# Kernel optimization log

Measured on AMD Instinct MI355X. Metric: run time of the kernel, lower is better.

Reference implementation:

```python
import jax, jax.numpy as jnp
import numpy as np

B, S, D = 4, 4096, 1024
H = 16
DH = D // H  # 64, required by the fused kernel


def setup_inputs() -> dict:
    key = jax.random.key(0)
    ks = jax.random.split(key, 5)
    scale = 1.0 / np.sqrt(D)  # xavier-ish init scale for square matrices
    return {
        "x": jax.random.normal(ks[0], (B, S, D), dtype=jnp.float32),
        "Wq": jax.random.normal(ks[1], (D, D), dtype=jnp.float32) * scale,
        "Wk": jax.random.normal(ks[2], (D, D), dtype=jnp.float32) * scale,
        "Wv": jax.random.normal(ks[3], (D, D), dtype=jnp.float32) * scale,
        "Wo": jax.random.normal(ks[4], (D, D), dtype=jnp.float32) * scale,
    }


def reference(x, Wq, Wk, Wv, Wo):
    # Fused QKV projection + linear (non-softmax) attention.
    # Q = x Wq, K = x Wk, V = x Wv, split into H heads of size DH.
    b, s, d = x.shape
    h, dh = H, d // H

    def to_heads(t):
        return t.reshape(b, s, h, dh).transpose(0, 2, 1, 3)  # [B,H,S,dh]

    q = to_heads(jnp.einsum("bsd,de->bse", x, Wq))
    k = to_heads(jnp.einsum("bsd,de->bse", x, Wk))
    v = to_heads(jnp.einsum("bsd,de->bse", x, Wv))

    # Linear attention: O(S * dh^2) per head, never materializes [S,S].
    # out = (1/sqrt(dh)) * Q @ (K^T V)
    scale = 1.0 / jnp.sqrt(jnp.asarray(dh, dtype=x.dtype))
    kv = jnp.einsum("bhsd,bhse->bhde", k, v)          # [B,H,dh,dh]
    out = jnp.einsum("bhsd,bhde->bhse", q, kv) * scale  # [B,H,S,dh]

    # kernel output [B,H,S,dh] -> transpose(1,2) -> view [B,S,D]
    out = out.transpose(0, 2, 1, 3).reshape(b, s, d)
    # out_proj: nn.Linear(D, D, bias=False) -> x @ W.T
    return jnp.einsum("bsd,ed->bse", out, Wo)
```

## Files before the change

### kernel.cpp

```cpp
#include <hip/hip_runtime.h>

typedef unsigned short u16;
typedef unsigned int u32;
typedef u16 u16x8 __attribute__((ext_vector_type(8)));
typedef u16 u16x4 __attribute__((ext_vector_type(4)));
typedef __bf16 bf16x8 __attribute__((ext_vector_type(8)));
typedef float f32x4 __attribute__((ext_vector_type(4)));

__device__ __forceinline__ u16 f2bf(float f) {
    u32 u = __builtin_bit_cast(u32, f);
    u32 r = (u + 0x7fffu + ((u >> 16) & 1u)) >> 16;
    return (u16)r;
}
__device__ __forceinline__ void async16(const u16* g, u16* lds_base) {
    __builtin_amdgcn_global_load_lds(
        (const __attribute__((address_space(1))) void*)g,
        (__attribute__((address_space(3))) void*)lds_base, 16, 0, 0);
}
__device__ __forceinline__ void storeC(float* p, float v) { *p = v; }
__device__ __forceinline__ void storeC(u16* p, float v)   { *p = f2bf(v); }

__global__ void cvt_f32_bf16(const float* __restrict__ in, u16* __restrict__ out, long n) {
    long idx = ((long)blockIdx.x * blockDim.x + threadIdx.x) * 8;
    if (idx >= n) return;
    float4 a = *(const float4*)(in + idx);
    float4 b = *(const float4*)(in + idx + 4);
    u16x8 o;
    o[0] = f2bf(a.x); o[1] = f2bf(a.y); o[2] = f2bf(a.z); o[3] = f2bf(a.w);
    o[4] = f2bf(b.x); o[5] = f2bf(b.y); o[6] = f2bf(b.z); o[7] = f2bf(b.w);
    *(u16x8*)(out + idx) = o;
}

__global__ void transpose_cvt(const float* __restrict__ W0, const float* __restrict__ W1,
                              u16* __restrict__ WT) {
    __shared__ float tile[32][33];
    const float* W = (blockIdx.z == 0) ? W0 : W1;
    int n0 = blockIdx.x * 32, k0 = blockIdx.y * 32;
    int tx = threadIdx.x, ty = threadIdx.y;
#pragma unroll
    for (int r = 0; r < 4; ++r)
        tile[ty + 8 * r][tx] = W[(size_t)(k0 + ty + 8 * r) * 1024 + n0 + tx];
    __syncthreads();
#pragma unroll
    for (int r = 0; r < 4; ++r) {
        int n = n0 + ty + 8 * r;
        WT[((size_t)blockIdx.z * 1024 + n) * 1024 + k0 + tx] = f2bf(tile[tx][ty + 8 * r]);
    }
}

#define BAR __builtin_amdgcn_s_barrier()
#define WAITLGK do { asm volatile("s_waitcnt lgkmcnt(0)" ::: "memory"); \
                     __builtin_amdgcn_sched_barrier(0); } while (0)
#define PRIO1 __builtin_amdgcn_s_setprio(1)
#define PRIO0 __builtin_amdgcn_s_setprio(0)
#define VM(n) asm volatile("s_waitcnt vmcnt(" #n ")" ::: "memory")

#define As SM[0]
#define Bs SM[1]

#define LDA(buf, mh) do { _Pragma("unroll") for (int mi = 0; mi < 4; ++mi) { \
    const int rA = (wm * 128 + (mh) * 64 + mi * 16 + frow) * 64; \
    aF[mi][0] = *(const bf16x8*)&As[buf][rA + xs0]; \
    aF[mi][1] = *(const bf16x8*)&As[buf][rA + xs1]; } } while (0)

#define LDB(buf, nh) do { _Pragma("unroll") for (int ni = 0; ni < 2; ++ni) { \
    const int rB = (wn * 64 + (nh) * 32 + ni * 16 + frow) * 64; \
    bF[(nh) * 2 + ni][0] = *(const bf16x8*)&Bs[buf][rB + xs0]; \
    bF[(nh) * 2 + ni][1] = *(const bf16x8*)&Bs[buf][rB + xs1]; } } while (0)

#define MFQ(mh, nh) do { _Pragma("unroll") for (int mi = 0; mi < 4; ++mi) \
  _Pragma("unroll") for (int ni = 0; ni < 2; ++ni) \
  _Pragma("unroll") for (int s = 0; s < 2; ++s) \
    acc[(mh) * 4 + mi][(nh) * 2 + ni] = __builtin_amdgcn_mfma_f32_16x16x32_bf16( \
        aF[mi][s], bF[(nh) * 2 + ni][s], acc[(mh) * 4 + mi][(nh) * 2 + ni], 0, 0, 0); } while (0)

#define TILE4(buf, S1, S2, S3, S4, WV) \
  LDA(buf, 0); LDB(buf, 0); S1; BAR; WAITLGK; PRIO1; MFQ(0, 0); PRIO0; BAR; \
  LDB(buf, 1); S2; BAR; WAITLGK; PRIO1; MFQ(0, 1); PRIO0; BAR; \
  LDA(buf, 1); S3; BAR; WAITLGK; PRIO1; MFQ(1, 1); PRIO0; BAR; \
  S4; BAR; WAITLGK; PRIO1; MFQ(1, 0); PRIO0; WV; BAR;

template <typename OutT, bool KVMODE>
__global__ __launch_bounds__(512, 2) void gemm8p(
    const u16* __restrict__ A, int lda,
    const u16* __restrict__ Bt, int ldb,
    OutT* __restrict__ Cq, int ldc, int K, int nTN,
    size_t btStrideB, u16* __restrict__ Kt, u16* __restrict__ Vt) {
    __shared__ u16 SM[2][2][256 * 64];
    const int tid = threadIdx.x;
    const int wid = tid >> 6, lane = tid & 63;
    const int wm = wid >> 2, wn = wid & 3;

    const int nwg = gridDim.x;
    const int orig = blockIdx.x;
    const int id = (orig & 7) * (nwg >> 3) + (orig >> 3);
    const size_t mBase = (size_t)(id / nTN) * 256;
    const size_t nBase = (size_t)(id % nTN) * 256;

    if (!KVMODE) Bt += (mBase >> 12) * btStrideB;

    const int srow = lane >> 3;
    const int scol = (((lane & 7) ^ (srow & 7)) * 8);

    auto stageH = [&](int buf, int isB, int h, int kt) {
        const u16* g = isB ? Bt : A;
        const int ld = isB ? ldb : lda;
        const size_t rb = isB ? nBase : mBase;
        u16* lds = isB ? Bs[buf] : As[buf];
#pragma unroll
        for (int j = 0; j < 2; ++j) {
            const int rowL = isB ? ((wid >> 1) * 64 + h * 32 + (wid & 1) * 16 + j * 8)
                                 : ((wid >> 2) * 128 + h * 64 + (wid & 3) * 16 + j * 8);
            async16(g + (rb + rowL + srow) * (size_t)ld + (size_t)kt * 64 + scol,
                    lds + rowL * 64);
        }
    };

    const int frow = lane & 15;
    const int xs0 = (((lane >> 4)) ^ (frow & 7)) * 8;
    const int xs1 = ((4 + (lane >> 4)) ^ (frow & 7)) * 8;

    f32x4 acc[8][4] = {};
    bf16x8 aF[4][2], bF[4][2];

#pragma unroll
    for (int h = 0; h < 2; ++h) { stageH(0, 0, h, 0); stageH(0, 1, h, 0); }
#pragma unroll
    for (int h = 0; h < 2; ++h) { stageH(1, 0, h, 1); stageH(1, 1, h, 1); }
    VM(8);
    BAR;

    const int np = K >> 7;
    for (int p = 0; p < np - 1; ++p) {
        const int k2 = 2 * p + 2, k3 = 2 * p + 3;
        TILE4(0, ,
              { stageH(0, 0, 0, k2); stageH(0, 1, 0, k2); },
              stageH(0, 1, 1, k2),
              stageH(0, 0, 1, k2),
              VM(8));
        TILE4(1, ,
              { stageH(1, 0, 0, k3); stageH(1, 1, 0, k3); },
              stageH(1, 1, 1, k3),
              stageH(1, 0, 1, k3),
              VM(8));
    }
    TILE4(0, , , , , VM(0));
    TILE4(1, , , , , );

    const int rb4 = (lane >> 4) * 4;
    const int cx = lane & 15;
    if (!KVMODE) {
#pragma unroll
        for (int m = 0; m < 8; ++m) {
#pragma unroll
            for (int n = 0; n < 4; ++n) {
                const size_t col = nBase + wn * 64 + n * 16 + cx;
#pragma unroll
                for (int r = 0; r < 4; ++r) {
                    const size_t row = mBase + wm * 128 + m * 16 + rb4 + r;
                    storeC(&Cq[row * (size_t)ldc + col], acc[m][n][r]);
                }
            }
        }
    } else {
        __syncthreads();
        u16* T = &SM[0][0][0];
        const int nLoc = (int)(nBase & 1023);
#pragma unroll
        for (int n = 0; n < 4; ++n) {
            const int colL = wn * 64 + n * 16 + cx;
#pragma unroll
            for (int m = 0; m < 8; ++m) {
                const int R = wm * 128 + m * 16 + rb4;
                u16x4 v;
                v[0] = f2bf(acc[m][n][0]); v[1] = f2bf(acc[m][n][1]);
                v[2] = f2bf(acc[m][n][2]); v[3] = f2bf(acc[m][n][3]);
                const int byteoff = colL * 512 + ((((R >> 3) ^ (colL & 31)) << 4) | ((R & 7) << 1));
                *(u16x4*)((char*)T + byteoff) = v;
            }
        }
        __syncthreads();
        const int b = (int)(mBase >> 12);
        u16* KV = ((nBase >> 10) == 0 ? Kt : Vt);
        const int j = lane & 31;
#pragma unroll
        for (int u = 0; u < 16; ++u) {
            const int iLoc = wid * 32 + u * 2 + (lane >> 5);
            const int byteoff = iLoc * 512 + ((j ^ (iLoc & 31)) << 4);
            const int gcol = nLoc + iLoc;
            u16* dst = KV + (((size_t)(b * 16 + (gcol >> 6)) * 64 + (gcol & 63)) << 12)
                          + (mBase & 4095) + j * 8;
            *(u16x8*)dst = *(const u16x8*)((char*)T + byteoff);
        }
    }
}

__global__ __launch_bounds__(256, 2) void gemm128(
    const u16* __restrict__ A, int lda,
    const u16* __restrict__ Bt, int ldb,
    u16* __restrict__ C, int ldc, int K) {
    __shared__ u16 A2[2][128 * 64];
    __shared__ u16 B2[2][128 * 64];
    const int tid = threadIdx.x, w = tid >> 6, lane = tid & 63;
    const int wr = w >> 1, wc = w & 1;
    const size_t mBase = (size_t)blockIdx.y * 128;
    const size_t nBase = (size_t)blockIdx.x * 128;
    const int lr = lane >> 3;
    const int scol = ((lane & 7) ^ lr) * 8;

    auto stage = [&](int buf, int kt) {
#pragma unroll
        for (int c = 0; c < 2; ++c) {
            const u16* g = c ? Bt : A;
            const int ld = c ? ldb : lda;
            const size_t rb = c ? nBase : mBase;
            u16* lds = c ? B2[buf] : A2[buf];
#pragma unroll
            for (int jj = 0; jj < 4; ++jj) {
                const int rowL = jj * 32 + w * 8;
                async16(g + (rb + rowL + lr) * (size_t)ld + (size_t)kt * 64 + scol,
                        lds + rowL * 64);
            }
        }
    };

    const int frow = lane & 15;
    const int xs0 = ((lane >> 4) ^ (frow & 7)) * 8;
    const int xs1 = ((4 + (lane >> 4)) ^ (frow & 7)) * 8;
    f32x4 acc[4][4] = {};

    stage(0, 0);
    __syncthreads();
    const int nk = K >> 6;
    for (int kt = 0; kt < nk; ++kt) {
        const int cur = kt & 1;
        if (kt + 1 < nk) stage(cur ^ 1, kt + 1);
        bf16x8 bF[4][2];
#pragma unroll
        for (int n = 0; n < 4; ++n) {
            const int rB = (wc * 64 + n * 16 + frow) * 64;
            bF[n][0] = *(const bf16x8*)&B2[cur][rB + xs0];
            bF[n][1] = *(const bf16x8*)&B2[cur][rB + xs1];
        }
#pragma unroll
        for (int m = 0; m < 4; ++m) {
            const int rA = (wr * 64 + m * 16 + frow) * 64;
            bf16x8 a0 = *(const bf16x8*)&A2[cur][rA + xs0];
            bf16x8 a1 = *(const bf16x8*)&A2[cur][rA + xs1];
#pragma unroll
            for (int n = 0; n < 4; ++n) {
                acc[m][n] = __builtin_amdgcn_mfma_f32_16x16x32_bf16(a0, bF[n][0], acc[m][n], 0, 0, 0);
                acc[m][n] = __builtin_amdgcn_mfma_f32_16x16x32_bf16(a1, bF[n][1], acc[m][n], 0, 0, 0);
            }
        }
        __syncthreads();
    }
    const int rb4 = (lane >> 4) * 4, cx = lane & 15;
#pragma unroll
    for (int m = 0; m < 4; ++m)
#pragma unroll
        for (int n = 0; n < 4; ++n) {
            const size_t col = nBase + wc * 64 + n * 16 + cx;
#pragma unroll
            for (int r = 0; r < 4; ++r)
                C[(mBase + wr * 64 + m * 16 + rb4 + r) * (size_t)ldc + col] = f2bf(acc[m][n][r]);
        }
}

__global__ __launch_bounds__(256, 2) void kv_gemm(
    const u16* __restrict__ Kt, const u16* __restrict__ Vt, float* __restrict__ P) {
    __shared__ u16 Ks[64 * 64];
    __shared__ u16 Vs[64 * 64];
    const int chunk = blockIdx.x, bh = blockIdx.y;
    const int tid = threadIdx.x, w = tid >> 6, lane = tid & 63;
    const int srow = lane >> 3;
    const int scol = ((lane & 7) ^ srow) * 8;
    const int frow = lane & 15;
    const int xs0 = ((lane >> 4) ^ (frow & 7)) * 8;
    const int xs1 = ((4 + (lane >> 4)) ^ (frow & 7)) * 8;
    const size_t base = (size_t)bh * 64 * 4096 + (size_t)chunk * 512;
    f32x4 acc[4] = {};
    for (int kk = 0; kk < 8; ++kk) {
        __syncthreads();
#pragma unroll
        for (int j = 0; j < 2; ++j) {
            const int row = w * 16 + j * 8;
            async16(Kt + base + (size_t)(row + srow) * 4096 + kk * 64 + scol, &Ks[row * 64]);
            async16(Vt + base + (size_t)(row + srow) * 4096 + kk * 64 + scol, &Vs[row * 64]);
        }
        asm volatile("s_waitcnt vmcnt(0)" ::: "memory");
        __syncthreads();
        bf16x8 a0 = *(const bf16x8*)&Ks[(w * 16 + frow) * 64 + xs0];
        bf16x8 a1 = *(const bf16x8*)&Ks[(w * 16 + frow) * 64 + xs1];
#pragma unroll
        for (int n = 0; n < 4; ++n) {
            bf16x8 b0 = *(const bf16x8*)&Vs[(n * 16 + frow) * 64 + xs0];
            bf16x8 b1 = *(const bf16x8*)&Vs[(n * 16 + frow) * 64 + xs1];
            acc[n] = __builtin_amdgcn_mfma_f32_16x16x32_bf16(a0, b0, acc[n], 0, 0, 0);
            acc[n] = __builtin_amdgcn_mfma_f32_16x16x32_bf16(a1, b1, acc[n], 0, 0, 0);
        }
    }
    const int rb4 = (lane >> 4) * 4, cx = lane & 15;
    float* p = P + ((size_t)chunk * 64 + bh) * 4096;
#pragma unroll
    for (int n = 0; n < 4; ++n)
#pragma unroll
        for (int r = 0; r < 4; ++r)
            p[(w * 16 + rb4 + r) * 64 + n * 16 + cx] = acc[n][r];
}

__global__ void kv_reduce(const float* __restrict__ P, u16* __restrict__ kvb) {
    const int bh = blockIdx.x, t = threadIdx.x;
    for (int idx = t; idx < 4096; idx += 256) {
        float s = 0.f;
#pragma unroll
        for (int c = 0; c < 8; ++c) s += P[((size_t)c * 64 + bh) * 4096 + idx];
        kvb[(size_t)bh * 4096 + idx] = f2bf(s * 0.125f);
    }
}

__global__ __launch_bounds__(256, 2) void w2_gemm(
    const u16* __restrict__ Wob, const u16* __restrict__ kvb, u16* __restrict__ W2t) {
    __shared__ u16 Aw[256 * 64];
    __shared__ u16 Bw[64 * 64];
    const int eT = blockIdx.x, h = blockIdx.y, b = blockIdx.z;
    const int tid = threadIdx.x, w = tid >> 6, lane = tid & 63;
    const int srow = lane >> 3;
    const int scol = ((lane & 7) ^ srow) * 8;
#pragma unroll
    for (int j = 0; j < 8; ++j) {
        const int row = w * 64 + j * 8;
        async16(Wob + (size_t)(eT * 256 + row + srow) * 1024 + h * 64 + scol, &Aw[row * 64]);
    }
#pragma unroll
    for (int j = 0; j < 2; ++j) {
        const int row = w * 16 + j * 8;
        async16(kvb + ((size_t)(b * 16 + h) * 64 + row + srow) * 64 + scol, &Bw[row * 64]);
    }
    asm volatile("s_waitcnt vmcnt(0)" ::: "memory");
    __syncthreads();
    const int frow = lane & 15;
    const int xs0 = ((lane >> 4) ^ (frow & 7)) * 8;
    const int xs1 = ((4 + (lane >> 4)) ^ (frow & 7)) * 8;
    f32x4 acc[4][4] = {};
#pragma unroll
    for (int m = 0; m < 4; ++m) {
        bf16x8 a0 = *(const bf16x8*)&Aw[(w * 64 + m * 16 + frow) * 64 + xs0];
        bf16x8 a1 = *(const bf16x8*)&Aw[(w * 64 + m * 16 + frow) * 64 + xs1];
#pragma unroll
        for (int n = 0; n < 4; ++n) {
            bf16x8 b0 = *(const bf16x8*)&Bw[(n * 16 + frow) * 64 + xs0];
            bf16x8 b1 = *(const bf16x8*)&Bw[(n * 16 + frow) * 64 + xs1];
            acc[m][n] = __builtin_amdgcn_mfma_f32_16x16x32_bf16(a0, b0, acc[m][n], 0, 0, 0);
            acc[m][n] = __builtin_amdgcn_mfma_f32_16x16x32_bf16(a1, b1, acc[m][n], 0, 0, 0);
        }
    }
    const int rb4 = (lane >> 4) * 4, cx = lane & 15;
    u16* out = W2t + (size_t)b * 1048576;
#pragma unroll
    for (int m = 0; m < 4; ++m)
#pragma unroll
        for (int n = 0; n < 4; ++n)
#pragma unroll
            for (int r = 0; r < 4; ++r)
                out[(size_t)(eT * 256 + w * 64 + m * 16 + rb4 + r) * 1024 + h * 64 + n * 16 + cx] =
                    f2bf(acc[m][n][r]);
}

extern "C" void kernel_launch(void* const* d_in, const int* in_sizes, int n_in,
                              void* d_out, int out_size, void* d_ws, size_t ws_size,
                              hipStream_t stream) {
    const float* x  = (const float*)d_in[0];
    const float* Wq = (const float*)d_in[1];
    const float* Wk = (const float*)d_in[2];
    const float* Wv = (const float*)d_in[3];
    const float* Wo = (const float*)d_in[4];
    float* out = (float*)d_out;
    char* ws = (char*)d_ws;

    u16*   xb    = (u16*)(ws);
    u16*   Kt    = (u16*)(ws + 33554432);
    u16*   Vt    = (u16*)(ws + 67108864);
    u16*   WkvT  = (u16*)(ws + 100663296);
    u16*   Wqb   = (u16*)(ws + 104857600);
    u16*   Wob   = (u16*)(ws + 106954752);
    float* Pkv   = (float*)(ws + 109051904);
    u16*   kvb   = (u16*)(ws + 117440512);
    u16*   W2t   = (u16*)(ws + 117964800);
    u16*   W3T   = (u16*)(ws + 126353408);

    cvt_f32_bf16<<<8192, 256, 0, stream>>>(x, xb, 16777216L);
    cvt_f32_bf16<<<512, 256, 0, stream>>>(Wq, Wqb, 1048576L);
    cvt_f32_bf16<<<512, 256, 0, stream>>>(Wo, Wob, 1048576L);
    transpose_cvt<<<dim3(32, 32, 2), dim3(32, 8), 0, stream>>>(Wk, Wv, WkvT);

    gemm8p<u16, true><<<512, 512, 0, stream>>>(xb, 1024, WkvT, 1024, (u16*)nullptr, 0,
                                               1024, 8, 0, Kt, Vt);

    kv_gemm<<<dim3(8, 64), 256, 0, stream>>>(Kt, Vt, Pkv);
    kv_reduce<<<64, 256, 0, stream>>>(Pkv, kvb);
    w2_gemm<<<dim3(4, 16, 4), 256, 0, stream>>>(Wob, kvb, W2t);

    gemm128<<<dim3(8, 32), 256, 0, stream>>>(W2t, 1024, Wqb, 1024, W3T, 1024, 1024);

    gemm8p<float, false><<<256, 512, 0, stream>>>(xb, 1024, W3T, 1024, out, 1024, 1024, 4,
                                                  1048576, nullptr, nullptr);
}
```

Measured before the change: 178.5 us.

## Software-pipeline LDS fragment loads across k-tiles and drop explicit lgkmcnt waits

Restructures the GEMM main loop so that the A-low and B-low fragments for the next k-tile are read from LDS during the current tile's last MFMA quadrant, using double-buffered register fragments (bL0/bL1). The explicit lgkmcnt(0) waits are removed in favour of compiler-inserted waits with sched barriers, and the vmcnt wait moves to an earlier point in each tile. The aim is to hide LDS read latency behind MFMA work and cut pipeline stalls, at the cost of more live registers and a more delicate barrier and buffer ordering.

```diff
diff --git a/kernel.cpp b/kernel.cpp
--- a/kernel.cpp
+++ b/kernel.cpp
@@ -49,8 +49,7 @@
 }
 
 #define BAR __builtin_amdgcn_s_barrier()
-#define WAITLGK do { asm volatile("s_waitcnt lgkmcnt(0)" ::: "memory"); \
-                     __builtin_amdgcn_sched_barrier(0); } while (0)
+#define SB0 __builtin_amdgcn_sched_barrier(0)
 #define PRIO1 __builtin_amdgcn_s_setprio(1)
 #define PRIO0 __builtin_amdgcn_s_setprio(0)
 #define VM(n) asm volatile("s_waitcnt vmcnt(" #n ")" ::: "memory")
@@ -58,27 +57,56 @@
 #define As SM[0]
 #define Bs SM[1]
 
-#define LDA(buf, mh) do { _Pragma("unroll") for (int mi = 0; mi < 4; ++mi) { \
-    const int rA = (wm * 128 + (mh) * 64 + mi * 16 + frow) * 64; \
-    aF[mi][0] = *(const bf16x8*)&As[buf][rA + xs0]; \
-    aF[mi][1] = *(const bf16x8*)&As[buf][rA + xs1]; } } while (0)
-
-#define LDB(buf, nh) do { _Pragma("unroll") for (int ni = 0; ni < 2; ++ni) { \
-    const int rB = (wn * 64 + (nh) * 32 + ni * 16 + frow) * 64; \
-    bF[(nh) * 2 + ni][0] = *(const bf16x8*)&Bs[buf][rB + xs0]; \
-    bF[(nh) * 2 + ni][1] = *(const bf16x8*)&Bs[buf][rB + xs1]; } } while (0)
-
-#define MFQ(mh, nh) do { _Pragma("unroll") for (int mi = 0; mi < 4; ++mi) \
+#define LDALO(buf) do { _Pragma("unroll") for (int mi = 0; mi < 4; ++mi) { \
+    const int rA = (wm * 128 + mi * 16 + frow) * 64; \
+    aLo[mi][0] = *(const bf16x8*)&As[buf][rA + xs0]; \
+    aLo[mi][1] = *(const bf16x8*)&As[buf][rA + xs1]; } } while (0)
+
+#define LDAHI(buf) do { _Pragma("unroll") for (int mi = 0; mi < 4; ++mi) { \
+    const int rA = (wm * 128 + 64 + mi * 16 + frow) * 64; \
+    aHi[mi][0] = *(const bf16x8*)&As[buf][rA + xs0]; \
+    aHi[mi][1] = *(const bf16x8*)&As[buf][rA + xs1]; } } while (0)
+
+#define LDBL(BL, buf) do { _Pragma("unroll") for (int ni = 0; ni < 2; ++ni) { \
+    const int rB = (wn * 64 + ni * 16 + frow) * 64; \
+    BL[ni][0] = *(const bf16x8*)&Bs[buf][rB + xs0]; \
+    BL[ni][1] = *(const bf16x8*)&Bs[buf][rB + xs1]; } } while (0)
+
+#define LDBHI(buf) do { _Pragma("unroll") for (int ni = 0; ni < 2; ++ni) { \
+    const int rB = (wn * 64 + 32 + ni * 16 + frow) * 64; \
+    bHi[ni][0] = *(const bf16x8*)&Bs[buf][rB + xs0]; \
+    bHi[ni][1] = *(const bf16x8*)&Bs[buf][rB + xs1]; } } while (0)
+
+#define MFQ00(BL) do { _Pragma("unroll") for (int mi = 0; mi < 4; ++mi) \
   _Pragma("unroll") for (int ni = 0; ni < 2; ++ni) \
   _Pragma("unroll") for (int s = 0; s < 2; ++s) \
-    acc[(mh) * 4 + mi][(nh) * 2 + ni] = __builtin_amdgcn_mfma_f32_16x16x32_bf16( \
-        aF[mi][s], bF[(nh) * 2 + ni][s], acc[(mh) * 4 + mi][(nh) * 2 + ni], 0, 0, 0); } while (0)
-
-#define TILE4(buf, S1, S2, S3, S4, WV) \
-  LDA(buf, 0); LDB(buf, 0); S1; BAR; WAITLGK; PRIO1; MFQ(0, 0); PRIO0; BAR; \
-  LDB(buf, 1); S2; BAR; WAITLGK; PRIO1; MFQ(0, 1); PRIO0; BAR; \
-  LDA(buf, 1); S3; BAR; WAITLGK; PRIO1; MFQ(1, 1); PRIO0; BAR; \
-  S4; BAR; WAITLGK; PRIO1; MFQ(1, 0); PRIO0; WV; BAR;
+    acc[mi][ni] = __builtin_amdgcn_mfma_f32_16x16x32_bf16(aLo[mi][s], BL[ni][s], acc[mi][ni], 0, 0, 0); } while (0)
+#define MFQ01 do { _Pragma("unroll") for (int mi = 0; mi < 4; ++mi) \
+  _Pragma("unroll") for (int ni = 0; ni < 2; ++ni) \
+  _Pragma("unroll") for (int s = 0; s < 2; ++s) \
+    acc[mi][2 + ni] = __builtin_amdgcn_mfma_f32_16x16x32_bf16(aLo[mi][s], bHi[ni][s], acc[mi][2 + ni], 0, 0, 0); } while (0)
+#define MFQ11 do { _Pragma("unroll") for (int mi = 0; mi < 4; ++mi) \
+  _Pragma("unroll") for (int ni = 0; ni < 2; ++ni) \
+  _Pragma("unroll") for (int s = 0; s < 2; ++s) \
+    acc[4 + mi][2 + ni] = __builtin_amdgcn_mfma_f32_16x16x32_bf16(aHi[mi][s], bHi[ni][s], acc[4 + mi][2 + ni], 0, 0, 0); } while (0)
+#define MFQ10(BL) do { _Pragma("unroll") for (int mi = 0; mi < 4; ++mi) \
+  _Pragma("unroll") for (int ni = 0; ni < 2; ++ni) \
+  _Pragma("unroll") for (int s = 0; s < 2; ++s) \
+    acc[4 + mi][ni] = __builtin_amdgcn_mfma_f32_16x16x32_bf16(aHi[mi][s], BL[ni][s], acc[4 + mi][ni], 0, 0, 0); } while (0)
+
+#define TILEP(buf, BLC, BLN, stg, kt2, look) do { \
+  LDBHI(buf); SB0; PRIO1; MFQ00(BLC); PRIO0; BAR; SB0; \
+  LDAHI(buf); \
+  if (stg) { stageH(buf, 0, 0, kt2); stageH(buf, 1, 0, kt2); } \
+  SB0; PRIO1; MFQ01; PRIO0; BAR; SB0; \
+  if (stg) stageH(buf, 1, 1, kt2); \
+  SB0; PRIO1; MFQ11; PRIO0; \
+  if (stg) { VM(6); } else { VM(0); } \
+  BAR; SB0; \
+  if (look) { LDALO((buf) ^ 1); LDBL(BLN, (buf) ^ 1); } \
+  if (stg) stageH(buf, 0, 1, kt2); \
+  SB0; PRIO1; MFQ10(BLC); PRIO0; BAR; SB0; \
+} while (0)
 
 template <typename OutT, bool KVMODE>
 __global__ __launch_bounds__(512, 2) void gemm8p(
@@ -121,31 +149,21 @@
     const int xs1 = ((4 + (lane >> 4)) ^ (frow & 7)) * 8;
 
     f32x4 acc[8][4] = {};
-    bf16x8 aF[4][2], bF[4][2];
+    bf16x8 aLo[4][2], aHi[4][2], bL0[2][2], bL1[2][2], bHi[2][2];
 
 #pragma unroll
     for (int h = 0; h < 2; ++h) { stageH(0, 0, h, 0); stageH(0, 1, h, 0); }
 #pragma unroll
     for (int h = 0; h < 2; ++h) { stageH(1, 0, h, 1); stageH(1, 1, h, 1); }
     VM(8);
-    BAR;
-
-    const int np = K >> 7;
-    for (int p = 0; p < np - 1; ++p) {
-        const int k2 = 2 * p + 2, k3 = 2 * p + 3;
-        TILE4(0, ,
-              { stageH(0, 0, 0, k2); stageH(0, 1, 0, k2); },
-              stageH(0, 1, 1, k2),
-              stageH(0, 0, 1, k2),
-              VM(8));
-        TILE4(1, ,
-              { stageH(1, 0, 0, k3); stageH(1, 1, 0, k3); },
-              stageH(1, 1, 1, k3),
-              stageH(1, 0, 1, k3),
-              VM(8));
-    }
-    TILE4(0, , , , , VM(0));
-    TILE4(1, , , , , );
+    BAR; SB0;
+    LDALO(0); LDBL(bL0, 0);
+
+    const int nt = K >> 6;
+    for (int t = 0; t < nt; t += 2) {
+        TILEP(0, bL0, bL1, (t + 2 < nt), t + 2, true);
+        TILEP(1, bL1, bL0, (t + 3 < nt), t + 3, (t + 2 < nt));
+    }
 
     const int rb4 = (lane >> 4) * 4;
     const int cx = lane & 15;
```

Measured after the change: 299.9 us. 1.68x slower.
